# Performance work log

Hardware: AMD Instinct MI355X
Metric: run time of the kernel (lower is better)

The kernel has to match this reference:

```python
import jax, jax.numpy as jnp
import numpy as np

DIM = 768
D_STATE = 16
D_INNER = 2 * DIM  # expand=2


def setup_inputs() -> dict:
    key = jax.random.key(0)
    k_x, k_in, k_conv, k_out = jax.random.split(key, 4)
    B, L = 1, 4096
    x = jax.random.normal(k_x, (B, L, DIM), dtype=jnp.float32)
    # torch Linear weight layout: [out_features, in_features]
    W_in = jax.random.normal(k_in, (3 * D_INNER + 2 * D_STATE, DIM), dtype=jnp.float32) * 0.02
    # depthwise conv1d kernel: [out_ch=d_inner, in_ch/groups=1, k=3]
    W_conv = jax.random.normal(k_conv, (D_INNER, 1, 3), dtype=jnp.float32) * 0.1
    W_out = jax.random.normal(k_out, (DIM, D_INNER), dtype=jnp.float32) * 0.02
    A_log = jnp.log(jnp.tile(jnp.arange(1, D_STATE + 1, dtype=jnp.float32), (D_INNER, 1)))
    D = jnp.ones((D_INNER,), dtype=jnp.float32)
    return {"x": x, "W_in": W_in, "W_conv": W_conv, "W_out": W_out, "A_log": A_log, "D": D}


def reference(x, W_in, W_conv, W_out, A_log, D):
    d_inner = W_conv.shape[0]
    d_state = A_log.shape[1]
    Bsz = x.shape[0]

    xz = x @ W_in.T  # [B, L, 3*d_inner + 2*d_state]
    x_inner, z, B_ssm, C_ssm, delta = jnp.split(
        xz, [d_inner, 2 * d_inner, 2 * d_inner + d_state, 2 * d_inner + 2 * d_state], axis=-1
    )

    # depthwise conv over sequence: [B, d_inner, L]
    xc = jax.lax.conv_general_dilated(
        x_inner.transpose(0, 2, 1), W_conv,
        window_strides=(1,), padding=[(1, 1)], feature_group_count=d_inner,
    ).transpose(0, 2, 1)  # back to [B, L, d_inner]
    xc = jax.nn.silu(xc)

    A = -jnp.exp(A_log)  # [d_inner, d_state]
    delta = jax.nn.softplus(delta)  # [B, L, d_inner]
    dA = jnp.exp(jnp.einsum('bld,dn->bldn', delta, A))           # [B, L, d_inner, d_state]
    dBx = jnp.einsum('bld,bln,bld->bldn', delta, B_ssm, xc)      # delta_B * x fused

    def step(h, inp):
        da_t, dbx_t, c_t = inp  # [B,d,n], [B,d,n], [B,n]
        h = da_t * h + dbx_t
        y_t = jnp.einsum('bdn,bn->bd', h, c_t)
        return h, y_t

    h0 = jnp.zeros((Bsz, d_inner, d_state), dtype=x.dtype)
    _, ys = jax.lax.scan(
        step, h0,
        (dA.transpose(1, 0, 2, 3), dBx.transpose(1, 0, 2, 3), C_ssm.transpose(1, 0, 2)),
    )  # ys: [L, B, d_inner]

    y = ys.transpose(1, 0, 2) + xc * D  # skip connection
    y = y * jax.nn.silu(z)
    return y @ W_out.T  # [B, L, dim]
```

## Files before the change

### kernel.cpp

```cpp
#include <hip/hip_runtime.h>
#include <hip/hip_bf16.h>
#include <math.h>

#define LSEQ   4096
#define DIM    768
#define DINNER 1536
#define DSTATE 16
#define NCOLS  4640
#define NCH    256
#define CLEN   16
#define NPAD   4736
#define DXW    1568

typedef _Float16 f16;
typedef __attribute__((ext_vector_type(4))) _Float16 f16x4;
typedef __attribute__((ext_vector_type(8))) _Float16 f16x8;
typedef __attribute__((ext_vector_type(4))) float f32x4;

__device__ __forceinline__ void gld_lds16(void* lds_dst, const void* gsrc) {
    __builtin_amdgcn_global_load_lds(
        (__attribute__((address_space(1))) void*)(gsrc),
        (__attribute__((address_space(3))) void*)(lds_dst), 16, 0, 0);
}

#define G1K    768
#define G1_NT  12
#define G1_BM  256
#define G1_BN  128
#define G1_RT  384
#define G1_LDSE (G1_RT * 64)

__global__ __launch_bounds__(512) void gemm1_pipe(const f16* __restrict__ A,
                                                  const f16* __restrict__ B,
                                                  float* __restrict__ C,
                                                  f16* __restrict__ Xb,
                                                  f16* __restrict__ Zb) {
    __shared__ __align__(16) f16 S[3 * G1_LDSE];

    const int P   = gridDim.x >> 3;
    const int idx = (blockIdx.x & 7) * P + (blockIdx.x >> 3);
    const int m0  = (idx & 15) * G1_BM;
    const int n0  = (idx >> 4) * G1_BN;

    const int tid  = threadIdx.x;
    const int w    = tid >> 6;
    const int lane = tid & 63;
    const int wr   = w >> 1;
    const int wc   = w & 1;
    const int m    = lane & 15;
    const int q    = lane >> 4;
    const int rl8  = lane >> 3;
    const int bsel = lane & 7;

    const f16* gb[6];
#pragma unroll
    for (int s = 0; s < 6; ++s) {
        const int rl  = (w + 8 * s) * 8 + rl8;
        const int blk = bsel ^ (rl & 7);
        gb[s] = (rl < G1_BM) ? A + (size_t)(m0 + rl) * G1K + blk * 8
                             : B + (size_t)(n0 + rl - G1_BM) * G1K + blk * 8;
    }

    f32x4 acc[4][4];
#pragma unroll
    for (int i = 0; i < 4; i++)
#pragma unroll
        for (int j = 0; j < 4; j++) acc[i][j] = (f32x4){0.f, 0.f, 0.f, 0.f};

    auto stg2 = [&](int kt, int s0) {
        f16* dst = S + (kt % 3) * G1_LDSE;
#pragma unroll
        for (int s = s0; s < s0 + 2; ++s)
            gld_lds16(dst + (w + 8 * s) * 512, gb[s] + kt * 64);
    };
    auto stg6 = [&](int kt) {
        f16* dst = S + (kt % 3) * G1_LDSE;
#pragma unroll
        for (int s = 0; s < 6; ++s)
            gld_lds16(dst + (w + 8 * s) * 512, gb[s] + kt * 64);
    };

    stg6(0);
    stg6(1);

#pragma unroll
    for (int kt = 0; kt < G1_NT; ++kt) {
        if (kt < G1_NT - 1) asm volatile("s_waitcnt vmcnt(6)" ::: "memory");
        else                asm volatile("s_waitcnt vmcnt(0)" ::: "memory");
        __builtin_amdgcn_s_barrier();
        const f16* As = S + (kt % 3) * G1_LDSE;
        const f16* Bs = As + G1_BM * 64;
        const bool pf = (kt + 2 < G1_NT);

        f16x8 af0[2][2], af2[2][2], bh0[2][2], bh2[2][2];

#pragma unroll
        for (int kk = 0; kk < 2; ++kk) {
            const int fo = (((q + 4 * kk) ^ (m & 7)) << 3);
#pragma unroll
            for (int i = 0; i < 2; ++i) {
                af0[kk][i] = *(const f16x8*)&As[(wr * 64 + i * 16 + m) * 64 + fo];
                bh0[kk][i] = *(const f16x8*)&Bs[(wc * 64 + i * 16 + m) * 64 + fo];
            }
        }
        if (pf) stg2(kt + 2, 0);
        __builtin_amdgcn_s_barrier();
        asm volatile("s_waitcnt lgkmcnt(0)" ::: "memory");
        __builtin_amdgcn_sched_barrier(0);
        __builtin_amdgcn_s_setprio(1);
#pragma unroll
        for (int kk = 0; kk < 2; ++kk)
#pragma unroll
            for (int i = 0; i < 2; ++i)
#pragma unroll
                for (int j = 0; j < 2; ++j)
                    acc[i][j] = __builtin_amdgcn_mfma_f32_16x16x32_f16(
                        af0[kk][i], bh0[kk][j], acc[i][j], 0, 0, 0);
        __builtin_amdgcn_s_setprio(0);

#pragma unroll
        for (int kk = 0; kk < 2; ++kk) {
            const int fo = (((q + 4 * kk) ^ (m & 7)) << 3);
#pragma unroll
            for (int j = 0; j < 2; ++j)
                bh2[kk][j] = *(const f16x8*)&Bs[(wc * 64 + (j + 2) * 16 + m) * 64 + fo];
        }
        if (pf) stg2(kt + 2, 2);
        __builtin_amdgcn_s_barrier();
        asm volatile("s_waitcnt lgkmcnt(0)" ::: "memory");
        __builtin_amdgcn_sched_barrier(0);
        __builtin_amdgcn_s_setprio(1);
#pragma unroll
        for (int kk = 0; kk < 2; ++kk)
#pragma unroll
            for (int i = 0; i < 2; ++i)
#pragma unroll
                for (int j = 0; j < 2; ++j)
                    acc[i][j + 2] = __builtin_amdgcn_mfma_f32_16x16x32_f16(
                        af0[kk][i], bh2[kk][j], acc[i][j + 2], 0, 0, 0);
        __builtin_amdgcn_s_setprio(0);

#pragma unroll
        for (int kk = 0; kk < 2; ++kk) {
            const int fo = (((q + 4 * kk) ^ (m & 7)) << 3);
#pragma unroll
            for (int i = 0; i < 2; ++i)
                af2[kk][i] = *(const f16x8*)&As[(wr * 64 + (i + 2) * 16 + m) * 64 + fo];
        }
        if (pf) stg2(kt + 2, 4);
        __builtin_amdgcn_s_barrier();
        asm volatile("s_waitcnt lgkmcnt(0)" ::: "memory");
        __builtin_amdgcn_sched_barrier(0);
        __builtin_amdgcn_s_setprio(1);
#pragma unroll
        for (int kk = 0; kk < 2; ++kk)
#pragma unroll
            for (int i = 0; i < 2; ++i)
#pragma unroll
                for (int j = 0; j < 2; ++j)
                    acc[i + 2][j] = __builtin_amdgcn_mfma_f32_16x16x32_f16(
                        af2[kk][i], bh0[kk][j], acc[i + 2][j], 0, 0, 0);
        __builtin_amdgcn_s_setprio(0);

        __builtin_amdgcn_s_setprio(1);
#pragma unroll
        for (int kk = 0; kk < 2; ++kk)
#pragma unroll
            for (int i = 0; i < 2; ++i)
#pragma unroll
                for (int j = 0; j < 2; ++j)
                    acc[i + 2][j + 2] = __builtin_amdgcn_mfma_f32_16x16x32_f16(
                        af2[kk][i], bh2[kk][j], acc[i + 2][j + 2], 0, 0, 0);
        __builtin_amdgcn_s_setprio(0);
    }

    if (n0 < DINNER) {
#pragma unroll
        for (int i = 0; i < 4; i++)
#pragma unroll
            for (int j = 0; j < 4; j++) {
                const int col  = n0 + wc * 64 + j * 16 + m;
                const int rowb = m0 + wr * 64 + i * 16 + q * 4;
#pragma unroll
                for (int r = 0; r < 4; r++)
                    Xb[(size_t)(rowb + r) * DINNER + col] = (f16)acc[i][j][r];
            }
        return;
    }
    if (n0 < 2 * DINNER) {
#pragma unroll
        for (int i = 0; i < 4; i++)
#pragma unroll
            for (int j = 0; j < 4; j++) {
                const int col  = n0 - DINNER + wc * 64 + j * 16 + m;
                const int rowb = m0 + wr * 64 + i * 16 + q * 4;
#pragma unroll
                for (int r = 0; r < 4; r++)
                    Zb[(size_t)(rowb + r) * DINNER + col] = (f16)acc[i][j][r];
            }
        return;
    }
#pragma unroll
    for (int i = 0; i < 4; i++)
#pragma unroll
        for (int j = 0; j < 4; j++) {
            const int col = n0 - 2 * DINNER + wc * 64 + j * 16 + m;
            if (col >= DXW) continue;
            const int rowb = m0 + wr * 64 + i * 16 + q * 4;
#pragma unroll
            for (int r = 0; r < 4; r++)
                C[(size_t)(rowb + r) * DXW + col] = acc[i][j][r];
        }
}

#define G2K    1536
#define G2_NT  24
#define G2_LDSE (128 * 64)

__global__ __launch_bounds__(256) void gemm2_pipe(const f16* __restrict__ A,
                                                  const f16* __restrict__ B,
                                                  float* __restrict__ C) {
    __shared__ __align__(16) f16 S[3 * G2_LDSE];

    const int P   = gridDim.x >> 3;
    const int idx = (blockIdx.x & 7) * P + (blockIdx.x >> 3);
    const int m0  = (idx / 12) * 64;
    const int n0  = (idx % 12) * 64;

    const int tid  = threadIdx.x;
    const int w    = tid >> 6;
    const int lane = tid & 63;
    const int wr   = w >> 1;
    const int wc   = w & 1;
    const int m    = lane & 15;
    const int q    = lane >> 4;
    const int rl8  = lane >> 3;
    const int bsel = lane & 7;

    const f16* gb[4];
#pragma unroll
    for (int s = 0; s < 4; ++s) {
        const int rl  = (w + 4 * s) * 8 + rl8;
        const int blk = bsel ^ (rl & 7);
        gb[s] = (rl < 64) ? A + (size_t)(m0 + rl) * G2K + blk * 8
                          : B + (size_t)(n0 + rl - 64) * G2K + blk * 8;
    }

    f32x4 acc[2][2];
#pragma unroll
    for (int i = 0; i < 2; i++)
#pragma unroll
        for (int j = 0; j < 2; j++) acc[i][j] = (f32x4){0.f, 0.f, 0.f, 0.f};

    auto stg = [&](int kt) {
        f16* dst = S + (kt % 3) * G2_LDSE;
#pragma unroll
        for (int s = 0; s < 4; ++s)
            gld_lds16(dst + (w + 4 * s) * 512, gb[s] + kt * 64);
    };

    stg(0);
    stg(1);

#pragma unroll
    for (int kt = 0; kt < G2_NT; ++kt) {
        if (kt < G2_NT - 1) asm volatile("s_waitcnt vmcnt(4)" ::: "memory");
        else                asm volatile("s_waitcnt vmcnt(0)" ::: "memory");
        __builtin_amdgcn_s_barrier();
        if (kt + 2 < G2_NT) stg(kt + 2);

        const f16* As = S + (kt % 3) * G2_LDSE;
        const f16* Bs = As + 64 * 64;

        f16x8 af[2][2], bh[2][2];
#pragma unroll
        for (int kk = 0; kk < 2; ++kk) {
            const int fo = (((q + 4 * kk) ^ (m & 7)) << 3);
#pragma unroll
            for (int i = 0; i < 2; ++i) {
                af[kk][i] = *(const f16x8*)&As[(wr * 32 + i * 16 + m) * 64 + fo];
                bh[kk][i] = *(const f16x8*)&Bs[(wc * 32 + i * 16 + m) * 64 + fo];
            }
        }
        asm volatile("s_waitcnt lgkmcnt(0)" ::: "memory");
        __builtin_amdgcn_sched_barrier(0);
        __builtin_amdgcn_s_setprio(1);
#pragma unroll
        for (int kk = 0; kk < 2; ++kk)
#pragma unroll
            for (int i = 0; i < 2; ++i)
#pragma unroll
                for (int j = 0; j < 2; ++j)
                    acc[i][j] = __builtin_amdgcn_mfma_f32_16x16x32_f16(
                        af[kk][i], bh[kk][j], acc[i][j], 0, 0, 0);
        __builtin_amdgcn_s_setprio(0);
    }

#pragma unroll
    for (int i = 0; i < 2; i++)
#pragma unroll
        for (int j = 0; j < 2; j++) {
            const int col  = n0 + wc * 32 + j * 16 + m;
            const int rowb = m0 + wr * 32 + i * 16 + q * 4;
#pragma unroll
            for (int r = 0; r < 4; r++)
                C[(size_t)(rowb + r) * DIM + col] = acc[i][j][r];
        }
}

#define E0 (LSEQ * DIM)
#define E1 (E0 + NPAD * DIM)
#define E2 (E1 + DIM * DINNER)

__global__ __launch_bounds__(256) void cvt_all(const float* __restrict__ x,
                                               const float* __restrict__ Wi,
                                               const float* __restrict__ Wo,
                                               f16* __restrict__ Ax,
                                               f16* __restrict__ Bw,
                                               f16* __restrict__ Bo) {
    int i = (blockIdx.x * 256 + threadIdx.x) * 4;
    if (i < E0) {
        float4 v = *(const float4*)(x + i);
        f16x4 o = {(f16)v.x, (f16)v.y, (f16)v.z, (f16)v.w};
        *(f16x4*)(Ax + i) = o;
    } else if (i < E1) {
        int e = i - E0;
        int n = e / DIM;
        if (n < NCOLS) {
            float4 v = *(const float4*)(Wi + e);
            f16x4 o = {(f16)v.x, (f16)v.y, (f16)v.z, (f16)v.w};
            *(f16x4*)(Bw + e) = o;
        } else {
            f16x4 o = {(f16)0.f, (f16)0.f, (f16)0.f, (f16)0.f};
            *(f16x4*)(Bw + e) = o;
        }
    } else if (i < E2) {
        int e = i - E1;
        float4 v = *(const float4*)(Wo + e);
        f16x4 o = {(f16)v.x, (f16)v.y, (f16)v.z, (f16)v.w};
        *(f16x4*)(Bo + e) = o;
    }
}

__global__ __launch_bounds__(256) void scan1_kernel(const float* __restrict__ Dxz,
                                                    const f16* __restrict__ Xb,
                                                    const float* __restrict__ Wc,
                                                    const float* __restrict__ A_log,
                                                    float* __restrict__ aprod,
                                                    float* __restrict__ hend) {
    __shared__ float Bs[CLEN * DSTATE];
    const int d  = blockIdx.x * 256 + threadIdx.x;
    const int c  = blockIdx.y;
    const int l0 = c * CLEN;
    for (int i = threadIdx.x; i < CLEN * DSTATE; i += 256)
        Bs[i] = Dxz[(size_t)(l0 + (i >> 4)) * DXW + (i & 15)];
    float Areg[DSTATE];
#pragma unroll
    for (int n = 0; n < DSTATE; n++) Areg[n] = -__expf(A_log[d * DSTATE + n]);
    const float w0 = Wc[d * 3 + 0], w1 = Wc[d * 3 + 1], w2 = Wc[d * 3 + 2];
    float xm = (l0 > 0) ? (float)Xb[(size_t)(l0 - 1) * DINNER + d] : 0.f;
    float x0 = (float)Xb[(size_t)l0 * DINNER + d];
    float ld_xp   = (float)Xb[(size_t)(l0 + 1) * DINNER + d];
    float ld_draw = Dxz[(size_t)l0 * DXW + 32 + d];
    __syncthreads();

    float h[DSTATE];
#pragma unroll
    for (int n = 0; n < DSTATE; n++) h[n] = 0.f;
    float S = 0.f;

    for (int t = 0; t < CLEN; t++) {
        const int l = l0 + t;
        float xp = ld_xp, draw = ld_draw;
        if (t + 1 < CLEN) {
            ld_xp   = (l + 2 < LSEQ) ? (float)Xb[(size_t)(l + 2) * DINNER + d] : 0.f;
            ld_draw = Dxz[(size_t)(l + 1) * DXW + 32 + d];
        }
        float v  = xm * w0 + x0 * w1 + xp * w2;
        float xcv = __fdividef(v, 1.f + __expf(-v));
        float dtv = (draw > 20.f) ? draw : __logf(1.f + __expf(draw));
        float u = dtv * xcv;
        S += dtv;
#pragma unroll
        for (int n = 0; n < DSTATE; n++) {
            float e = __expf(dtv * Areg[n]);
            h[n] = e * h[n] + u * Bs[t * DSTATE + n];
        }
        xm = x0; x0 = xp;
    }
#pragma unroll
    for (int n = 0; n < DSTATE; n++) {
        size_t idx = ((size_t)c * DSTATE + n) * DINNER + d;
        aprod[idx] = __expf(S * Areg[n]);
        hend[idx]  = h[n];
    }
}

__global__ __launch_bounds__(256) void scan2_kernel(float* __restrict__ aphi,
                                                    const float* __restrict__ hend) {
    const int g = blockIdx.x * 256 + threadIdx.x;
    const size_t S = (size_t)DSTATE * DINNER;
    float aA[4], eA[4], aB[4], eB[4];
#pragma unroll
    for (int k = 0; k < 4; ++k) {
        aA[k] = aphi[g + (size_t)k * S];
        eA[k] = hend[g + (size_t)k * S];
    }
    float h = 0.f;
    for (int c = 0; c < NCH; c += 8) {
#pragma unroll
        for (int k = 0; k < 4; ++k) {
            aB[k] = aphi[g + (size_t)(c + 4 + k) * S];
            eB[k] = hend[g + (size_t)(c + 4 + k) * S];
        }
#pragma unroll
        for (int k = 0; k < 4; ++k) {
            aphi[g + (size_t)(c + k) * S] = h;
            h = aA[k] * h + eA[k];
        }
        if (c + 8 < NCH) {
#pragma unroll
            for (int k = 0; k < 4; ++k) {
                aA[k] = aphi[g + (size_t)(c + 8 + k) * S];
                eA[k] = hend[g + (size_t)(c + 8 + k) * S];
            }
        }
#pragma unroll
        for (int k = 0; k < 4; ++k) {
            aphi[g + (size_t)(c + 4 + k) * S] = h;
            h = aB[k] * h + eB[k];
        }
    }
}

__global__ __launch_bounds__(256) void scan3_kernel(const float* __restrict__ Dxz,
                                                    const f16* __restrict__ Xb,
                                                    const f16* __restrict__ Zb,
                                                    const float* __restrict__ Wc,
                                                    const float* __restrict__ A_log,
                                                    const float* __restrict__ hinit,
                                                    const float* __restrict__ Dp,
                                                    f16* __restrict__ Ay) {
    __shared__ float Bs[CLEN * DSTATE];
    __shared__ float Cs[CLEN * DSTATE];
    const int d  = blockIdx.x * 256 + threadIdx.x;
    const int c  = blockIdx.y;
    const int l0 = c * CLEN;
    for (int i = threadIdx.x; i < CLEN * DSTATE; i += 256) {
        size_t roff = (size_t)(l0 + (i >> 4)) * DXW;
        Bs[i] = Dxz[roff + (i & 15)];
        Cs[i] = Dxz[roff + 16 + (i & 15)];
    }
    float Areg[DSTATE];
#pragma unroll
    for (int n = 0; n < DSTATE; n++) Areg[n] = -__expf(A_log[d * DSTATE + n]);
    float h[DSTATE];
#pragma unroll
    for (int n = 0; n < DSTATE; n++)
        h[n] = hinit[((size_t)c * DSTATE + n) * DINNER + d];
    const float Dv = Dp[d];
    const float w0 = Wc[d * 3 + 0], w1 = Wc[d * 3 + 1], w2 = Wc[d * 3 + 2];
    float xm = (l0 > 0) ? (float)Xb[(size_t)(l0 - 1) * DINNER + d] : 0.f;
    float x0 = (float)Xb[(size_t)l0 * DINNER + d];
    float ld_xp   = (float)Xb[(size_t)(l0 + 1) * DINNER + d];
    float ld_draw = Dxz[(size_t)l0 * DXW + 32 + d];
    float ld_z    = (float)Zb[(size_t)l0 * DINNER + d];
    __syncthreads();

    for (int t = 0; t < CLEN; t++) {
        const int l = l0 + t;
        float xp = ld_xp, draw = ld_draw, zv = ld_z;
        if (t + 1 < CLEN) {
            ld_xp   = (l + 2 < LSEQ) ? (float)Xb[(size_t)(l + 2) * DINNER + d] : 0.f;
            ld_draw = Dxz[(size_t)(l + 1) * DXW + 32 + d];
            ld_z    = (float)Zb[(size_t)(l + 1) * DINNER + d];
        }
        float v  = xm * w0 + x0 * w1 + xp * w2;
        float xcv = __fdividef(v, 1.f + __expf(-v));
        float dtv = (draw > 20.f) ? draw : __logf(1.f + __expf(draw));
        float u = dtv * xcv;
        float y = 0.f;
#pragma unroll
        for (int n = 0; n < DSTATE; n++) {
            float e = __expf(dtv * Areg[n]);
            h[n] = e * h[n] + u * Bs[t * DSTATE + n];
            y += h[n] * Cs[t * DSTATE + n];
        }
        float sz = __fdividef(zv, 1.f + __expf(-zv));
        Ay[(size_t)l * DINNER + d] = (f16)((y + xcv * Dv) * sz);
        xm = x0; x0 = xp;
    }
}

extern "C" void kernel_launch(void* const* d_in, const int* in_sizes, int n_in,
                              void* d_out, int out_size, void* d_ws, size_t ws_size,
                              hipStream_t stream) {
    const float* x     = (const float*)d_in[0];
    const float* W_in  = (const float*)d_in[1];
    const float* W_conv= (const float*)d_in[2];
    const float* W_out = (const float*)d_in[3];
    const float* A_log = (const float*)d_in[4];
    const float* Dp    = (const float*)d_in[5];
    float* out = (float*)d_out;

    float* ws  = (float*)d_ws;
    float* Dxz = ws;
    float* ap  = Dxz + (size_t)LSEQ * DXW;
    float* he  = ap + (size_t)NCH * DSTATE * DINNER;
    f16* Ax = (f16*)(he + (size_t)NCH * DSTATE * DINNER);
    f16* Ay = Ax + (size_t)LSEQ * DIM;
    f16* Bw = Ay + (size_t)LSEQ * DINNER;
    f16* Bo = Bw + (size_t)NPAD * DIM;
    f16* Zb = Bo + (size_t)DIM * DINNER;
    f16* Xb = Zb + (size_t)LSEQ * DINNER;

    cvt_all<<<E2 / 1024, 256, 0, stream>>>(x, W_in, W_out, Ax, Bw, Bo);

    gemm1_pipe<<<592, 512, 0, stream>>>(Ax, Bw, Dxz, Xb, Zb);

    scan1_kernel<<<dim3(DINNER / 256, NCH), 256, 0, stream>>>(
        Dxz, Xb, W_conv, A_log, ap, he);
    scan2_kernel<<<(DINNER * DSTATE) / 256, 256, 0, stream>>>(ap, he);
    scan3_kernel<<<dim3(DINNER / 256, NCH), 256, 0, stream>>>(
        Dxz, Xb, Zb, W_conv, A_log, ap, Dp, Ay);

    gemm2_pipe<<<768, 256, 0, stream>>>(Ay, Bo, out);
}
```

Before: 237.6 us.

## Store per-chunk delta sums instead of decay products and regroup GEMM1 tile order

scan1 now writes one summed-delta value per chunk and channel instead of 16 per-state decay products, and scan2 recomputes each decay with exp(S*A), writing carry-in states to a separate buffer rather than overwriting in place. This cuts the intermediate traffic written by scan1 and read by scan2. scan2's prefetch depth goes from 4 to 8 chunks per buffer. The GEMM1 block-to-tile mapping now groups 8 M-tiles with every N-tile inside each partition, which is meant to improve L2 reuse of the A rows at the cost of some integer division.

```diff
diff --git a/kernel.cpp b/kernel.cpp
--- a/kernel.cpp
+++ b/kernel.cpp
@@ -39,8 +39,10 @@
 
     const int P   = gridDim.x >> 3;
     const int idx = (blockIdx.x & 7) * P + (blockIdx.x >> 3);
-    const int m0  = (idx & 15) * G1_BM;
-    const int n0  = (idx >> 4) * G1_BN;
+    const int sm  = idx / 296;
+    const int rem = idx - sm * 296;
+    const int m0  = (sm * 8 + (rem & 7)) * G1_BM;
+    const int n0  = (rem >> 3) * G1_BN;
 
     const int tid  = threadIdx.x;
     const int w    = tid >> 6;
@@ -346,7 +348,7 @@
                                                     const f16* __restrict__ Xb,
                                                     const float* __restrict__ Wc,
                                                     const float* __restrict__ A_log,
-                                                    float* __restrict__ aprod,
+                                                    float* __restrict__ Sb,
                                                     float* __restrict__ hend) {
     __shared__ float Bs[CLEN * DSTATE];
     const int d  = blockIdx.x * 256 + threadIdx.x;
@@ -388,47 +390,50 @@
         }
         xm = x0; x0 = xp;
     }
-#pragma unroll
-    for (int n = 0; n < DSTATE; n++) {
-        size_t idx = ((size_t)c * DSTATE + n) * DINNER + d;
-        aprod[idx] = __expf(S * Areg[n]);
-        hend[idx]  = h[n];
-    }
-}
-
-__global__ __launch_bounds__(256) void scan2_kernel(float* __restrict__ aphi,
-                                                    const float* __restrict__ hend) {
+    Sb[(size_t)c * DINNER + d] = S;
+#pragma unroll
+    for (int n = 0; n < DSTATE; n++)
+        hend[((size_t)c * DSTATE + n) * DINNER + d] = h[n];
+}
+
+__global__ __launch_bounds__(256) void scan2_kernel(const float* __restrict__ Sb,
+                                                    const float* __restrict__ A_log,
+                                                    const float* __restrict__ hend,
+                                                    float* __restrict__ hinit) {
     const int g = blockIdx.x * 256 + threadIdx.x;
+    const int n = g / DINNER;
+    const int d = g - n * DINNER;
+    const float Ar = -__expf(A_log[d * DSTATE + n]);
     const size_t S = (size_t)DSTATE * DINNER;
-    float aA[4], eA[4], aB[4], eB[4];
-#pragma unroll
-    for (int k = 0; k < 4; ++k) {
-        aA[k] = aphi[g + (size_t)k * S];
+    float sA[8], eA[8], sB[8], eB[8];
+#pragma unroll
+    for (int k = 0; k < 8; ++k) {
+        sA[k] = Sb[(size_t)k * DINNER + d];
         eA[k] = hend[g + (size_t)k * S];
     }
     float h = 0.f;
-    for (int c = 0; c < NCH; c += 8) {
-#pragma unroll
-        for (int k = 0; k < 4; ++k) {
-            aB[k] = aphi[g + (size_t)(c + 4 + k) * S];
-            eB[k] = hend[g + (size_t)(c + 4 + k) * S];
-        }
-#pragma unroll
-        for (int k = 0; k < 4; ++k) {
-            aphi[g + (size_t)(c + k) * S] = h;
-            h = aA[k] * h + eA[k];
-        }
-        if (c + 8 < NCH) {
-#pragma unroll
-            for (int k = 0; k < 4; ++k) {
-                aA[k] = aphi[g + (size_t)(c + 8 + k) * S];
-                eA[k] = hend[g + (size_t)(c + 8 + k) * S];
+    for (int c = 0; c < NCH; c += 16) {
+#pragma unroll
+        for (int k = 0; k < 8; ++k) {
+            sB[k] = Sb[(size_t)(c + 8 + k) * DINNER + d];
+            eB[k] = hend[g + (size_t)(c + 8 + k) * S];
+        }
+#pragma unroll
+        for (int k = 0; k < 8; ++k) {
+            hinit[g + (size_t)(c + k) * S] = h;
+            h = __expf(sA[k] * Ar) * h + eA[k];
+        }
+        if (c + 16 < NCH) {
+#pragma unroll
+            for (int k = 0; k < 8; ++k) {
+                sA[k] = Sb[(size_t)(c + 16 + k) * DINNER + d];
+                eA[k] = hend[g + (size_t)(c + 16 + k) * S];
             }
         }
 #pragma unroll
-        for (int k = 0; k < 4; ++k) {
-            aphi[g + (size_t)(c + 4 + k) * S] = h;
-            h = aB[k] * h + eB[k];
+        for (int k = 0; k < 8; ++k) {
+            hinit[g + (size_t)(c + 8 + k) * S] = h;
+            h = __expf(sB[k] * Ar) * h + eB[k];
         }
     }
 }
@@ -505,9 +510,10 @@
 
     float* ws  = (float*)d_ws;
     float* Dxz = ws;
-    float* ap  = Dxz + (size_t)LSEQ * DXW;
-    float* he  = ap + (size_t)NCH * DSTATE * DINNER;
-    f16* Ax = (f16*)(he + (size_t)NCH * DSTATE * DINNER);
+    float* hi  = Dxz + (size_t)LSEQ * DXW;
+    float* he  = hi + (size_t)NCH * DSTATE * DINNER;
+    float* Sb  = he + (size_t)NCH * DSTATE * DINNER;
+    f16* Ax = (f16*)(Sb + (size_t)NCH * DINNER);
     f16* Ay = Ax + (size_t)LSEQ * DIM;
     f16* Bw = Ay + (size_t)LSEQ * DINNER;
     f16* Bo = Bw + (size_t)NPAD * DIM;
@@ -519,10 +525,10 @@
     gemm1_pipe<<<592, 512, 0, stream>>>(Ax, Bw, Dxz, Xb, Zb);
 
     scan1_kernel<<<dim3(DINNER / 256, NCH), 256, 0, stream>>>(
-        Dxz, Xb, W_conv, A_log, ap, he);
-    scan2_kernel<<<(DINNER * DSTATE) / 256, 256, 0, stream>>>(ap, he);
+        Dxz, Xb, W_conv, A_log, Sb, he);
+    scan2_kernel<<<(DINNER * DSTATE) / 256, 256, 0, stream>>>(Sb, A_log, he, hi);
     scan3_kernel<<<dim3(DINNER / 256, NCH), 256, 0, stream>>>(
-        Dxz, Xb, Zb, W_conv, A_log, ap, Dp, Ay);
+        Dxz, Xb, Zb, W_conv, A_log, hi, Dp, Ay);
 
     gemm2_pipe<<<768, 256, 0, stream>>>(Ay, Bo, out);
 }
```

Result: no change. 241.8 us (+1.8%).
